# Performance work log

Measured on AMD Instinct MI355X. Metric: run time of the kernel, lower is better.

Reference implementation:

```python
import jax, jax.numpy as jnp
import numpy as np

N = 1024      # number of spans
D = 512       # span embedding dim (input_dim = 3*D)
H = 150       # hidden_dim
WIN = 250     # antecedent window from spans[ix-250:ix]


def setup_inputs() -> dict:
    key = jax.random.key(0)
    ks = jax.random.split(key, 8)
    return {
        "g": jax.random.normal(ks[0], (N, D), jnp.float32),
        "sm": jax.random.normal(ks[1], (N,), jnp.float32),
        "W1": jax.random.normal(ks[2], (3 * D, H), jnp.float32) * (1.0 / np.sqrt(3 * D)),
        "b1": jax.random.normal(ks[3], (H,), jnp.float32) * 0.01,
        "W2": jax.random.normal(ks[4], (H, H), jnp.float32) * (1.0 / np.sqrt(H)),
        "b2": jax.random.normal(ks[5], (H,), jnp.float32) * 0.01,
        "W3": jax.random.normal(ks[6], (H, 1), jnp.float32) * (1.0 / np.sqrt(H)),
        "b3": jax.random.normal(ks[7], (1,), jnp.float32) * 0.01,
    }


def reference(g, sm, W1, b1, W2, b2, W3, b3):
    n, d = g.shape
    # matching the in-order iteration over spans[ix-250:ix]
    j = jnp.arange(n)[:, None] - WIN + jnp.arange(WIN)[None, :]
    valid = j >= 0
    jc = jnp.clip(j, 0)

    # pair feature is cat([g_i, g_j, g_i*g_j]); split W1 so we can factor the first GEMM
    W1a, W1b, W1c = jnp.split(W1, 3, axis=0)            # each [D, H]
    gi_term = g @ W1a                                    # [N, H]
    gj_term = (g @ W1b)[jc]
    prod_term = jnp.einsum('nwd,dh->nwh', g[:, None, :] * g[jc], W1c)

    h = jax.nn.relu(gi_term[:, None, :] + gj_term + prod_term + b1)
    h = jax.nn.relu(h @ W2 + b2)
    s = (h @ W3 + b3)[..., 0]

    sij = sm[:, None] + sm[jc] + s                       # sm_i + sm_j + s_a
    sij = jnp.where(valid, sij, 0.0)                     # mask out-of-range antecedents
    eps = jnp.zeros((n, 1), g.dtype)                     # trailing epsilon = 0
    return jnp.concatenate([sij, eps], axis=1)
```

## Files before the change

kernel.cpp:

```cpp
#include <hip/hip_runtime.h>

typedef __attribute__((ext_vector_type(8))) short short8;
typedef __attribute__((ext_vector_type(4))) float f32x4;

#define NSPAN 1024
#define DDIM  512
#define HDIM  150
#define HPAD  160
#define WINW  250
#define OUTW  251

#define B1_OFF0 0
#define B1_OFF1 10240
#define A1_OFF0 20480
#define A1_OFF1 28672
#define GI_OFF  36864
#define SMEM_BYTES 40960

__device__ __forceinline__ unsigned short f2bf(float x) {
  union { float f; unsigned int u; } v; v.f = x;
  return (unsigned short)((v.u + 0x7fffu + ((v.u >> 16) & 1u)) >> 16);
}

__device__ __forceinline__ unsigned int cvtpk(float a, float b) {
  unsigned int r;
  asm("v_cvt_pk_bf16_f32 %0, %1, %2" : "=v"(r) : "v"(a), "v"(b));
  return r;
}

__device__ __forceinline__ void gload_lds16(const void* g, void* l) {
  __builtin_amdgcn_global_load_lds(
      (const __attribute__((address_space(1))) unsigned int*)g,
      (__attribute__((address_space(3))) unsigned int*)l, 16, 0, 0);
}

__global__ __launch_bounds__(192) void prep_gemm(
    const float* __restrict__ g, const float* __restrict__ W1,
    const float* __restrict__ b1, float* __restrict__ pre1,
    float* __restrict__ gjb)
{
  __shared__ __align__(16) float gs[2 * DDIM];
  const int grp = blockIdx.x >> 1;
  const int which = blockIdx.x & 1;
  const int i0 = grp << 1;
  for (int idx = threadIdx.x; idx < (2 * DDIM / 4); idx += 192)
    ((float4*)gs)[idx] = ((const float4*)(g + (size_t)i0 * DDIM))[idx];
  __syncthreads();
  const int n = threadIdx.x;
  float a0 = 0.f, a1 = 0.f;
  if (n < HDIM) {
    const float* Wp = W1 + (size_t)which * DDIM * HDIM + n;
#pragma unroll 8
    for (int d = 0; d < DDIM; ++d) {
      float w = Wp[(size_t)d * HDIM];
      a0 += gs[d] * w;
      a1 += gs[DDIM + d] * w;
    }
  }
  if (n < HPAD) {
    float* dst = which ? gjb : pre1;
    float add = (which == 0 && n < HDIM) ? b1[n] : 0.f;
    float v0 = (n < HDIM) ? (a0 + add) : 0.f;
    float v1 = (n < HDIM) ? (a1 + add) : 0.f;
    dst[(size_t)i0 * HPAD + n] = v0;
    dst[(size_t)(i0 + 1) * HPAD + n] = v1;
  }
}

__global__ void prep_misc(const float* __restrict__ W1, const float* __restrict__ W2,
                          const float* __restrict__ W3,
                          unsigned short* __restrict__ w1cT,
                          unsigned short* __restrict__ w2T,
                          float* __restrict__ w3p)
{
  int id = blockIdx.x * 256 + threadIdx.x;
  if (id < HPAD * DDIM) {
    int d = id / HPAD, n = id % HPAD;
    float v = (n < HDIM) ? W1[(size_t)(2 * DDIM + d) * HDIM + n] : 0.f;
    w1cT[(size_t)n * DDIM + d] = f2bf(v);
  } else if (id < HPAD * DDIM + HPAD * HPAD) {
    int id2 = id - HPAD * DDIM;
    int k = id2 / HPAD, n = id2 % HPAD;
    float v = (n < HDIM && k < HDIM) ? W2[(size_t)k * HDIM + n] : 0.f;
    w2T[(size_t)n * HPAD + k] = f2bf(v);
  } else if (id < HPAD * DDIM + HPAD * HPAD + HPAD) {
    int n = id - HPAD * DDIM - HPAD * HPAD;
    w3p[n] = (n < HDIM) ? W3[n] : 0.f;
  }
}

__global__ __launch_bounds__(256, 3) void pair_main(
    const float* __restrict__ g, const float* __restrict__ sm,
    const float* __restrict__ pre1, const float* __restrict__ gjb,
    const unsigned short* __restrict__ w1cT, const unsigned short* __restrict__ w2T,
    const float* __restrict__ w3p, const float* __restrict__ b2,
    const float* __restrict__ b3, float* __restrict__ out)
{
  __shared__ __align__(16) char smem[SMEM_BYTES];
  const int tid = threadIdx.x;
  const int lane = tid & 63;
  const int wv = tid >> 6;
  const int l15 = lane & 15;
  const int lq = lane >> 4;
  const int i = blockIdx.x >> 1;
  const int mbase = (blockIdx.x & 1) << 7;

  float* giL = (float*)(smem + GI_OFF);
  if (tid < 128)
    ((float4*)giL)[tid] = ((const float4*)(g + (size_t)i * DDIM))[tid];

  const int r_s = tid >> 1;
  const int kh = (tid & 1) << 4;
  const int j_s = i - WINW + mbase + r_s;
  const int jc_s = j_s < 0 ? 0 : (j_s > NSPAN - 1 ? NSPAN - 1 : j_s);
  const float4* gj4 = (const float4*)(g + (size_t)jc_s * DDIM);
  const int swA = ((r_s >> 1) & 7) << 4;
  const int stA0 = (((r_s << 6) + (kh << 1)) ^ swA);
  const int stA1 = (((r_s << 6) + (kh << 1) + 16) ^ swA);

  unsigned int bsrc[3];
#pragma unroll
  for (int t = 0; t < 3; ++t) {
    int b = wv * 2560 + (t << 10) + (lane << 4);
    int m = b >> 7;
    int bp = b ^ ((m & 7) << 4);
    int n = bp >> 6, o = bp & 63;
    bsrc[t] = (unsigned int)(n * 1024 + o);
  }

  int xa[2];
#pragma unroll
  for (int mt = 0; mt < 2; ++mt) {
    int row = (wv << 5) + (mt << 4) + l15;
    xa[mt] = ((row << 6) + (lq << 4)) ^ (((row >> 1) & 7) << 4);
  }
  int xb[10];
#pragma unroll
  for (int nt = 0; nt < 10; ++nt) {
    int nr = (nt << 4) + l15;
    xb[nt] = ((nr << 6) + (lq << 4)) ^ (((nr >> 1) & 7) << 4);
  }

  f32x4 acc[2][10];
#pragma unroll
  for (int mt = 0; mt < 2; ++mt)
#pragma unroll
    for (int nt = 0; nt < 10; ++nt)
      acc[mt][nt] = (f32x4){0.f, 0.f, 0.f, 0.f};

  const char* w1cB = (const char*)w1cT;
  __syncthreads();

  for (int s = 0; s < 16; ++s) {
    const int k0 = s << 5;
    char* a1b = smem + ((s & 1) ? A1_OFF1 : A1_OFF0);
    char* b1b = smem + ((s & 1) ? B1_OFF1 : B1_OFF0);

    {
      char* ldsw = b1b + wv * 2560;
      gload_lds16(w1cB + bsrc[0] + (k0 << 1), ldsw);
      gload_lds16(w1cB + bsrc[1] + (k0 << 1), ldsw + 1024);
      if (lane < 32)
        gload_lds16(w1cB + bsrc[2] + (k0 << 1), ldsw + 2048);
    }
    {
      const int fb = (k0 + kh) >> 2;
      float4 x0 = gj4[fb], x1 = gj4[fb + 1], x2 = gj4[fb + 2], x3 = gj4[fb + 3];
      const float4* gi4 = ((const float4*)giL) + fb;
      float4 y0 = gi4[0], y1 = gi4[1], y2 = gi4[2], y3 = gi4[3];
      uint4 w0, w1;
      w0.x = cvtpk(x0.x * y0.x, x0.y * y0.y);
      w0.y = cvtpk(x0.z * y0.z, x0.w * y0.w);
      w0.z = cvtpk(x1.x * y1.x, x1.y * y1.y);
      w0.w = cvtpk(x1.z * y1.z, x1.w * y1.w);
      w1.x = cvtpk(x2.x * y2.x, x2.y * y2.y);
      w1.y = cvtpk(x2.z * y2.z, x2.w * y2.w);
      w1.z = cvtpk(x3.x * y3.x, x3.y * y3.y);
      w1.w = cvtpk(x3.z * y3.z, x3.w * y3.w);
      *(uint4*)(a1b + stA0) = w0;
      *(uint4*)(a1b + stA1) = w1;
    }
    __syncthreads();
    short8 a0 = *(const short8*)(a1b + xa[0]);
    short8 a1 = *(const short8*)(a1b + xa[1]);
#pragma unroll
    for (int nt = 0; nt < 10; ++nt) {
      short8 bb = *(const short8*)(b1b + xb[nt]);
      acc[0][nt] = __builtin_amdgcn_mfma_f32_16x16x32_bf16(a0, bb, acc[0][nt], 0, 0, 0);
      acc[1][nt] = __builtin_amdgcn_mfma_f32_16x16x32_bf16(a1, bb, acc[1][nt], 0, 0, 0);
    }
  }
  __syncthreads();

  float p1v[10];
#pragma unroll
  for (int nt = 0; nt < 10; ++nt)
    p1v[nt] = pre1[(size_t)i * HPAD + (nt << 4) + l15];

#pragma unroll
  for (int mt = 0; mt < 2; ++mt) {
#pragma unroll
    for (int rr = 0; rr < 4; ++rr) {
      const int row = (wv << 5) + (mt << 4) + (lq << 2) + rr;
      int j = i - WINW + mbase + row;
      j = j < 0 ? 0 : (j > NSPAN - 1 ? NSPAN - 1 : j);
      const float* gjr = gjb + (size_t)j * HPAD;
      const int sw = ((row + (row >> 2)) & 3) << 4;
      const int rb = row * 320;
#pragma unroll
      for (int np = 0; np < 5; ++np) {
        const int n0 = np << 1, n1 = n0 + 1;
        float v0 = fmaxf(acc[mt][n0][rr] + p1v[n0] + gjr[(n0 << 4) + l15], 0.f);
        float v1 = fmaxf(acc[mt][n1][rr] + p1v[n1] + gjr[(n1 << 4) + l15], 0.f);
        unsigned int u = cvtpk(v0, v1);
        *(unsigned short*)(smem + ((rb + (((n0 << 4) + l15) << 1)) ^ sw)) = (unsigned short)u;
        *(unsigned short*)(smem + ((rb + (((n1 << 4) + l15) << 1)) ^ sw)) = (unsigned short)(u >> 16);
      }
    }
  }

  int ya[2];
#pragma unroll
  for (int mt = 0; mt < 2; ++mt) {
    int row = (wv << 5) + (mt << 4) + l15;
    ya[mt] = ((row * 320) + (lq << 4)) ^ (((row + (row >> 2)) & 3) << 4);
  }

  __syncthreads();

#pragma unroll
  for (int mt = 0; mt < 2; ++mt)
#pragma unroll
    for (int nt = 0; nt < 10; ++nt)
      acc[mt][nt] = (f32x4){0.f, 0.f, 0.f, 0.f};

#pragma unroll
  for (int c = 0; c < 5; ++c) {
    short8 a0 = *(const short8*)(smem + ya[0] + (c << 6));
    short8 a1 = *(const short8*)(smem + ya[1] + (c << 6));
#pragma unroll
    for (int nt = 0; nt < 10; ++nt) {
      short8 bb = *(const short8*)(w2T + (size_t)((nt << 4) + l15) * HPAD + (c << 5) + (lq << 3));
      acc[0][nt] = __builtin_amdgcn_mfma_f32_16x16x32_bf16(a0, bb, acc[0][nt], 0, 0, 0);
      acc[1][nt] = __builtin_amdgcn_mfma_f32_16x16x32_bf16(a1, bb, acc[1][nt], 0, 0, 0);
    }
  }
  __syncthreads();

  float w3v[10], b2v[10];
#pragma unroll
  for (int nt = 0; nt < 10; ++nt) {
    int nn = (nt << 4) + l15;
    w3v[nt] = w3p[nn];
    b2v[nt] = (nn < HDIM) ? b2[nn] : 0.f;
  }
  float* sL = (float*)smem;
#pragma unroll
  for (int mt = 0; mt < 2; ++mt) {
#pragma unroll
    for (int rr = 0; rr < 4; ++rr) {
      float part = 0.f;
#pragma unroll
      for (int nt = 0; nt < 10; ++nt) {
        float h2 = fmaxf(acc[mt][nt][rr] + b2v[nt], 0.f);
        part = fmaf(h2, w3v[nt], part);
      }
      part += __shfl_xor(part, 1);
      part += __shfl_xor(part, 2);
      part += __shfl_xor(part, 4);
      part += __shfl_xor(part, 8);
      if (l15 == 0)
        sL[(wv << 5) + (mt << 4) + (lq << 2) + rr] = part;
    }
  }
  __syncthreads();

  if (tid < 128) {
    const int rg = mbase + tid;
    if (rg <= WINW) {
      const int j = i - WINW + rg;
      float v = 0.f;
      if (rg < WINW && j >= 0)
        v = sL[tid] + b3[0] + sm[i] + sm[j];
      out[(size_t)i * OUTW + rg] = v;
    }
  }
}

extern "C" void kernel_launch(void* const* d_in, const int* in_sizes, int n_in,
                              void* d_out, int out_size, void* d_ws, size_t ws_size,
                              hipStream_t stream) {
  const float* g  = (const float*)d_in[0];
  const float* sm = (const float*)d_in[1];
  const float* W1 = (const float*)d_in[2];
  const float* b1 = (const float*)d_in[3];
  const float* W2 = (const float*)d_in[4];
  const float* b2 = (const float*)d_in[5];
  const float* W3 = (const float*)d_in[6];
  const float* b3 = (const float*)d_in[7];
  float* out = (float*)d_out;

  char* ws = (char*)d_ws;
  float* pre1          = (float*)ws;
  float* gjb           = (float*)(ws + 655360);
  unsigned short* w1cT = (unsigned short*)(ws + 1310720);
  unsigned short* w2T  = (unsigned short*)(ws + 1474560);
  float* w3p           = (float*)(ws + 1525760);

  prep_gemm<<<1024, 192, 0, stream>>>(g, W1, b1, pre1, gjb);
  prep_misc<<<(HPAD * DDIM + HPAD * HPAD + HPAD + 255) / 256, 256, 0, stream>>>(
      W1, W2, W3, w1cT, w2T, w3p);
  pair_main<<<2048, 256, 0, stream>>>(g, sm, pre1, gjb, w1cT, w2T, w3p, b2, b3, out);
}
```

Baseline: 191.5 us.

## Build pair-product MFMA A-fragments in registers and prefetch next K-step

```diff
diff --git a/kernel.cpp b/kernel.cpp
--- a/kernel.cpp
+++ b/kernel.cpp
@@ -12,10 +12,8 @@
 
 #define B1_OFF0 0
 #define B1_OFF1 10240
-#define A1_OFF0 20480
-#define A1_OFF1 28672
-#define GI_OFF  36864
-#define SMEM_BYTES 40960
+#define SL_OFF  40960
+#define SMEM_BYTES 41472
 
 __device__ __forceinline__ unsigned short f2bf(float x) {
   union { float f; unsigned int u; } v; v.f = x;
@@ -105,18 +103,14 @@
   const int i = blockIdx.x >> 1;
   const int mbase = (blockIdx.x & 1) << 7;
 
-  float* giL = (float*)(smem + GI_OFF);
-  if (tid < 128)
-    ((float4*)giL)[tid] = ((const float4*)(g + (size_t)i * DDIM))[tid];
-
-  const int r_s = tid >> 1;
-  const int kh = (tid & 1) << 4;
-  const int j_s = i - WINW + mbase + r_s;
-  const int jc_s = j_s < 0 ? 0 : (j_s > NSPAN - 1 ? NSPAN - 1 : j_s);
-  const float4* gj4 = (const float4*)(g + (size_t)jc_s * DDIM);
-  const int swA = ((r_s >> 1) & 7) << 4;
-  const int stA0 = (((r_s << 6) + (kh << 1)) ^ swA);
-  const int stA1 = (((r_s << 6) + (kh << 1) + 16) ^ swA);
+  const int row0 = mbase + (wv << 5) + l15;
+  int j0 = i - WINW + row0;
+  j0 = j0 < 0 ? 0 : (j0 > NSPAN - 1 ? NSPAN - 1 : j0);
+  int j1 = i - WINW + row0 + 16;
+  j1 = j1 < 0 ? 0 : (j1 > NSPAN - 1 ? NSPAN - 1 : j1);
+  const float* gjr0 = g + (size_t)j0 * DDIM + (lq << 3);
+  const float* gjr1 = g + (size_t)j1 * DDIM + (lq << 3);
+  const float* giR  = g + (size_t)i * DDIM + (lq << 3);
 
   unsigned int bsrc[3];
 #pragma unroll
@@ -128,12 +122,6 @@
     bsrc[t] = (unsigned int)(n * 1024 + o);
   }
 
-  int xa[2];
-#pragma unroll
-  for (int mt = 0; mt < 2; ++mt) {
-    int row = (wv << 5) + (mt << 4) + l15;
-    xa[mt] = ((row << 6) + (lq << 4)) ^ (((row >> 1) & 7) << 4);
-  }
   int xb[10];
 #pragma unroll
   for (int nt = 0; nt < 10; ++nt) {
@@ -149,48 +137,68 @@
       acc[mt][nt] = (f32x4){0.f, 0.f, 0.f, 0.f};
 
   const char* w1cB = (const char*)w1cT;
+
+  {
+    char* ldsw = smem + B1_OFF0 + wv * 2560;
+    gload_lds16(w1cB + bsrc[0], ldsw);
+    gload_lds16(w1cB + bsrc[1], ldsw + 1024);
+    if (lane < 32) gload_lds16(w1cB + bsrc[2], ldsw + 2048);
+  }
+  uint4 aC0, aC1;
+  {
+    float4 x0 = *(const float4*)gjr0, x1 = *(const float4*)(gjr0 + 4);
+    float4 y0 = *(const float4*)gjr1, y1 = *(const float4*)(gjr1 + 4);
+    float4 g0 = *(const float4*)giR,  g1 = *(const float4*)(giR + 4);
+    aC0.x = cvtpk(x0.x * g0.x, x0.y * g0.y);
+    aC0.y = cvtpk(x0.z * g0.z, x0.w * g0.w);
+    aC0.z = cvtpk(x1.x * g1.x, x1.y * g1.y);
+    aC0.w = cvtpk(x1.z * g1.z, x1.w * g1.w);
+    aC1.x = cvtpk(y0.x * g0.x, y0.y * g0.y);
+    aC1.y = cvtpk(y0.z * g0.z, y0.w * g0.w);
+    aC1.z = cvtpk(y1.x * g1.x, y1.y * g1.y);
+    aC1.w = cvtpk(y1.z * g1.z, y1.w * g1.w);
+  }
   __syncthreads();
 
+#pragma unroll 2
   for (int s = 0; s < 16; ++s) {
-    const int k0 = s << 5;
-    char* a1b = smem + ((s & 1) ? A1_OFF1 : A1_OFF0);
-    char* b1b = smem + ((s & 1) ? B1_OFF1 : B1_OFF0);
-
-    {
-      char* ldsw = b1b + wv * 2560;
-      gload_lds16(w1cB + bsrc[0] + (k0 << 1), ldsw);
-      gload_lds16(w1cB + bsrc[1] + (k0 << 1), ldsw + 1024);
-      if (lane < 32)
-        gload_lds16(w1cB + bsrc[2] + (k0 << 1), ldsw + 2048);
-    }
-    {
-      const int fb = (k0 + kh) >> 2;
-      float4 x0 = gj4[fb], x1 = gj4[fb + 1], x2 = gj4[fb + 2], x3 = gj4[fb + 3];
-      const float4* gi4 = ((const float4*)giL) + fb;
-      float4 y0 = gi4[0], y1 = gi4[1], y2 = gi4[2], y3 = gi4[3];
-      uint4 w0, w1;
-      w0.x = cvtpk(x0.x * y0.x, x0.y * y0.y);
-      w0.y = cvtpk(x0.z * y0.z, x0.w * y0.w);
-      w0.z = cvtpk(x1.x * y1.x, x1.y * y1.y);
-      w0.w = cvtpk(x1.z * y1.z, x1.w * y1.w);
-      w1.x = cvtpk(x2.x * y2.x, x2.y * y2.y);
-      w1.y = cvtpk(x2.z * y2.z, x2.w * y2.w);
-      w1.z = cvtpk(x3.x * y3.x, x3.y * y3.y);
-      w1.w = cvtpk(x3.z * y3.z, x3.w * y3.w);
-      *(uint4*)(a1b + stA0) = w0;
-      *(uint4*)(a1b + stA1) = w1;
-    }
-    __syncthreads();
-    short8 a0 = *(const short8*)(a1b + xa[0]);
-    short8 a1 = *(const short8*)(a1b + xa[1]);
+    char* bcur = smem + ((s & 1) ? B1_OFF1 : B1_OFF0);
+    char* bnxt = smem + ((s & 1) ? B1_OFF0 : B1_OFF1);
+
+    if (s < 15) {
+      const int kn = (s + 1) << 6;
+      char* ldsw = bnxt + wv * 2560;
+      gload_lds16(w1cB + bsrc[0] + kn, ldsw);
+      gload_lds16(w1cB + bsrc[1] + kn, ldsw + 1024);
+      if (lane < 32) gload_lds16(w1cB + bsrc[2] + kn, ldsw + 2048);
+    }
+    float4 x0, x1, y0, y1, g0, g1;
+    if (s < 15) {
+      const int kf = (s + 1) << 5;
+      x0 = *(const float4*)(gjr0 + kf); x1 = *(const float4*)(gjr0 + kf + 4);
+      y0 = *(const float4*)(gjr1 + kf); y1 = *(const float4*)(gjr1 + kf + 4);
+      g0 = *(const float4*)(giR + kf);  g1 = *(const float4*)(giR + kf + 4);
+    }
+    short8 a0 = *(short8*)&aC0;
+    short8 a1 = *(short8*)&aC1;
 #pragma unroll
     for (int nt = 0; nt < 10; ++nt) {
-      short8 bb = *(const short8*)(b1b + xb[nt]);
+      short8 bb = *(const short8*)(bcur + xb[nt]);
       acc[0][nt] = __builtin_amdgcn_mfma_f32_16x16x32_bf16(a0, bb, acc[0][nt], 0, 0, 0);
       acc[1][nt] = __builtin_amdgcn_mfma_f32_16x16x32_bf16(a1, bb, acc[1][nt], 0, 0, 0);
     }
-  }
-  __syncthreads();
+    if (s < 15) {
+      aC0.x = cvtpk(x0.x * g0.x, x0.y * g0.y);
+      aC0.y = cvtpk(x0.z * g0.z, x0.w * g0.w);
+      aC0.z = cvtpk(x1.x * g1.x, x1.y * g1.y);
+      aC0.w = cvtpk(x1.z * g1.z, x1.w * g1.w);
+      aC1.x = cvtpk(y0.x * g0.x, y0.y * g0.y);
+      aC1.y = cvtpk(y0.z * g0.z, y0.w * g0.w);
+      aC1.z = cvtpk(y1.x * g1.x, y1.y * g1.y);
+      aC1.w = cvtpk(y1.z * g1.z, y1.w * g1.w);
+    }
+    __syncthreads();
+  }
 
   float p1v[10];
 #pragma unroll
@@ -226,8 +234,6 @@
     ya[mt] = ((row * 320) + (lq << 4)) ^ (((row + (row >> 2)) & 3) << 4);
   }
 
-  __syncthreads();
-
 #pragma unroll
   for (int mt = 0; mt < 2; ++mt)
 #pragma unroll
@@ -245,7 +251,6 @@
       acc[1][nt] = __builtin_amdgcn_mfma_f32_16x16x32_bf16(a1, bb, acc[1][nt], 0, 0, 0);
     }
   }
-  __syncthreads();
 
   float w3v[10], b2v[10];
 #pragma unroll
@@ -254,7 +259,7 @@
     w3v[nt] = w3p[nn];
     b2v[nt] = (nn < HDIM) ? b2[nn] : 0.f;
   }
-  float* sL = (float*)smem;
+  float* sL = (float*)(smem + SL_OFF);
 #pragma unroll
   for (int mt = 0; mt < 2; ++mt) {
 #pragma unroll
```

Measured after the change: 209.7 us. 1.09x slower.
